# Optimization experiments

Measured on AMD Instinct MI355X. Metric: run time of the kernel, lower is better.

## Reference

```python
import jax, jax.numpy as jnp
import numpy as np

N_NODES = 12288
N_EDGES = 393216
LATENT = 128
EDGE_F = 4


def setup_inputs() -> dict:
    key = jax.random.key(0)
    k1, k2, k3, k4 = jax.random.split(key, 4)
    z = jax.random.normal(k1, (N_NODES, LATENT), dtype=jnp.float32)
    edge_index = jax.random.randint(k2, (2, N_EDGES), 0, N_NODES, dtype=jnp.int64)
    edge_attr = jax.random.normal(k3, (N_EDGES, EDGE_F), dtype=jnp.float32)
    W = jax.random.normal(k4, (1, 2 * LATENT), dtype=jnp.float32) * (1.0 / np.sqrt(2 * LATENT))
    b = jnp.zeros((1,), dtype=jnp.float32)
    return {"z": z, "edge_index": edge_index, "edge_attr": edge_attr, "W": W, "b": b}


def reference(z, edge_index, edge_attr, W, b):
    # z: [N, D], edge_index: [2, E], edge_attr: [E, F], W: [1, 2D], b: [1]
    num_nodes = z.shape[0]
    row, col = edge_index[0], edge_index[1]
    # gather node embeddings per edge and apply tiny linear: [E, 2D] @ [2D, 1]
    edge_features = jnp.concatenate([z[row], z[col]], axis=1)
    specified_edge_probs = (edge_features @ W.T + b)[:, 0]  # [E]
    # scatter edge probs into dense NxN (indexed assignment, like torch)
    full_edge_probs = jnp.zeros((num_nodes, num_nodes), dtype=z.dtype).at[row, col].set(specified_edge_probs)
    # to_dense_adj scatter-adds edge_attr -> [N, N, F]; sum(dim=3) commutes, so add summed attr
    adj = jnp.zeros((num_nodes, num_nodes), dtype=edge_attr.dtype).at[row, col].add(edge_attr.sum(axis=1))
    return adj + full_edge_probs
```

## Files before the change

kernel.cpp:

```cpp
#include <hip/hip_runtime.h>

#define N_NODES 12288
#define N_EDGES 393216
#define LATENT  128

#define E_BITS  19
#define E_MASK  ((1u << E_BITS) - 1u)

__device__ __forceinline__ unsigned int hash32(unsigned int key) {
    key ^= key >> 16; key *= 0x85ebca6bu;
    key ^= key >> 13; key *= 0xc2b2ae35u;
    key ^= key >> 16;
    return key;
}

__global__ void node_dots(const float* __restrict__ z, const float* __restrict__ W,
                          float* __restrict__ s1, float* __restrict__ s2) {
    int node = (int)((blockIdx.x * blockDim.x + threadIdx.x) >> 6);
    int lane = (int)(threadIdx.x & 63);
    if (node >= N_NODES) return;
    const float* zr = z + (size_t)node * LATENT;
    float a  = zr[lane];
    float bb = zr[lane + 64];
    float p1 = a * W[lane]       + bb * W[lane + 64];
    float p2 = a * W[lane + 128] + bb * W[lane + 192];
    #pragma unroll
    for (int off = 32; off > 0; off >>= 1) {
        p1 += __shfl_down(p1, off, 64);
        p2 += __shfl_down(p2, off, 64);
    }
    if (lane == 0) { s1[node] = p1; s2[node] = p2; }
}

__global__ void build_table(const int* __restrict__ ei,
                            unsigned long long* __restrict__ table,
                            unsigned int tab_mask) {
    int e = (int)(blockIdx.x * blockDim.x + threadIdx.x);
    if (e >= N_EDGES) return;
    unsigned int r = (unsigned int)ei[e];
    unsigned int c = (unsigned int)ei[e + N_EDGES];
    unsigned int key = r * (unsigned int)N_NODES + c;
    unsigned long long packed = (((unsigned long long)(key + 1u)) << E_BITS) | (unsigned int)e;
    unsigned int h = hash32(key) & tab_mask;
    for (;;) {
        unsigned long long old = atomicCAS(&table[h], 0ull, packed);
        if (old == 0ull) break;
        if ((unsigned int)(old >> E_BITS) == key + 1u) {
            atomicMax(&table[h], packed);
            break;
        }
        h = (h + 1u) & tab_mask;
    }
}

__global__ void scatter_edges(const int* __restrict__ ei, const float* __restrict__ ea,
                              const float* __restrict__ s1, const float* __restrict__ s2,
                              const float* __restrict__ bptr,
                              const unsigned long long* __restrict__ table,
                              unsigned int tab_mask,
                              float* __restrict__ out) {
    int e = (int)(blockIdx.x * blockDim.x + threadIdx.x);
    if (e >= N_EDGES) return;
    unsigned int r = (unsigned int)ei[e];
    unsigned int c = (unsigned int)ei[e + N_EDGES];
    unsigned int key = r * (unsigned int)N_NODES + c;
    float4 a4 = ((const float4*)ea)[e];
    float val = a4.x + a4.y + a4.z + a4.w;

    unsigned int h = hash32(key) & tab_mask;
    for (;;) {
        unsigned long long entry = table[h];
        if (entry == 0ull) break;
        if ((unsigned int)(entry >> E_BITS) == key + 1u) {
            if ((unsigned int)(entry & E_MASK) == (unsigned int)e)
                val += s1[r] + s2[c] + bptr[0];
            break;
        }
        h = (h + 1u) & tab_mask;
    }
    atomicAdd(&out[(size_t)key], val);
}

extern "C" void kernel_launch(void* const* d_in, const int* in_sizes, int n_in,
                              void* d_out, int out_size, void* d_ws, size_t ws_size,
                              hipStream_t stream) {
    const float* z  = (const float*)d_in[0];
    const int*   ei = (const int*)d_in[1];
    const float* ea = (const float*)d_in[2];
    const float* W  = (const float*)d_in[3];
    const float* b  = (const float*)d_in[4];
    float* out = (float*)d_out;

    char* ws = (char*)d_ws;
    float* s1 = (float*)ws;
    float* s2 = (float*)(ws + (size_t)N_NODES * sizeof(float));
    unsigned long long* table = (unsigned long long*)(ws + 2ull * N_NODES * sizeof(float));
    size_t head = 2ull * N_NODES * sizeof(float);

    int bits = 19;
    while (bits < 22 && head + (8ull << (bits + 1)) <= ws_size) bits++;
    unsigned int tab_mask = (1u << bits) - 1u;
    size_t tab_bytes = 8ull << bits;

    hipMemsetAsync(d_out, 0, (size_t)out_size * sizeof(float), stream);
    hipMemsetAsync(table, 0, tab_bytes, stream);

    node_dots<<<N_NODES / 4, 256, 0, stream>>>(z, W, s1, s2);
    build_table<<<N_EDGES / 256, 256, 0, stream>>>(ei, table, tab_mask);
    scatter_edges<<<N_EDGES / 256, 256, 0, stream>>>(ei, ea, s1, s2, b, table, tab_mask, out);
}
```

Measured before the change: 670.3 us.

## Fuse attr scatter into table build and add probs via table sweep

The edge-attribute atomic scatter moves into the hash-table build kernel. The old second per-edge pass, which re-read the edges and re-probed the hash table, is replaced by a linear sweep over the table that adds each unique edge's probability to the output with a plain read-modify-write. This drops one pass over edge_index and edge_attr along with the random table probes. The table is capped at 2^20 entries, which shortens the sweep but raises load factor and collision chains compared with the old larger table.

```diff
diff --git a/kernel.cpp b/kernel.cpp
--- a/kernel.cpp
+++ b/kernel.cpp
@@ -32,14 +32,18 @@
     if (lane == 0) { s1[node] = p1; s2[node] = p2; }
 }
 
-__global__ void build_table(const int* __restrict__ ei,
-                            unsigned long long* __restrict__ table,
-                            unsigned int tab_mask) {
+__global__ void edge_pass(const int* __restrict__ ei, const float* __restrict__ ea,
+                          unsigned long long* __restrict__ table, unsigned int tab_mask,
+                          float* __restrict__ out) {
     int e = (int)(blockIdx.x * blockDim.x + threadIdx.x);
     if (e >= N_EDGES) return;
     unsigned int r = (unsigned int)ei[e];
     unsigned int c = (unsigned int)ei[e + N_EDGES];
     unsigned int key = r * (unsigned int)N_NODES + c;
+
+    float4 a4 = ((const float4*)ea)[e];
+    atomicAdd(&out[(size_t)key], a4.x + a4.y + a4.z + a4.w);
+
     unsigned long long packed = (((unsigned long long)(key + 1u)) << E_BITS) | (unsigned int)e;
     unsigned int h = hash32(key) & tab_mask;
     for (;;) {
@@ -53,32 +57,17 @@
     }
 }
 
-__global__ void scatter_edges(const int* __restrict__ ei, const float* __restrict__ ea,
-                              const float* __restrict__ s1, const float* __restrict__ s2,
-                              const float* __restrict__ bptr,
-                              const unsigned long long* __restrict__ table,
-                              unsigned int tab_mask,
-                              float* __restrict__ out) {
-    int e = (int)(blockIdx.x * blockDim.x + threadIdx.x);
-    if (e >= N_EDGES) return;
-    unsigned int r = (unsigned int)ei[e];
-    unsigned int c = (unsigned int)ei[e + N_EDGES];
-    unsigned int key = r * (unsigned int)N_NODES + c;
-    float4 a4 = ((const float4*)ea)[e];
-    float val = a4.x + a4.y + a4.z + a4.w;
-
-    unsigned int h = hash32(key) & tab_mask;
-    for (;;) {
-        unsigned long long entry = table[h];
-        if (entry == 0ull) break;
-        if ((unsigned int)(entry >> E_BITS) == key + 1u) {
-            if ((unsigned int)(entry & E_MASK) == (unsigned int)e)
-                val += s1[r] + s2[c] + bptr[0];
-            break;
-        }
-        h = (h + 1u) & tab_mask;
-    }
-    atomicAdd(&out[(size_t)key], val);
+__global__ void add_probs(const unsigned long long* __restrict__ table, unsigned int tab_n,
+                          const float* __restrict__ s1, const float* __restrict__ s2,
+                          const float* __restrict__ bptr, float* __restrict__ out) {
+    unsigned int i = blockIdx.x * blockDim.x + threadIdx.x;
+    if (i >= tab_n) return;
+    unsigned long long entry = table[i];
+    if (entry == 0ull) return;
+    unsigned int key = (unsigned int)(entry >> E_BITS) - 1u;
+    unsigned int r = key / (unsigned int)N_NODES;
+    unsigned int c = key - r * (unsigned int)N_NODES;
+    out[(size_t)key] += s1[r] + s2[c] + bptr[0];
 }
 
 extern "C" void kernel_launch(void* const* d_in, const int* in_sizes, int n_in,
@@ -97,15 +86,15 @@
     unsigned long long* table = (unsigned long long*)(ws + 2ull * N_NODES * sizeof(float));
     size_t head = 2ull * N_NODES * sizeof(float);
 
-    int bits = 19;
-    while (bits < 22 && head + (8ull << (bits + 1)) <= ws_size) bits++;
-    unsigned int tab_mask = (1u << bits) - 1u;
+    int bits = (head + (8ull << 20) <= ws_size) ? 20 : 19;
+    unsigned int tab_n = 1u << bits;
+    unsigned int tab_mask = tab_n - 1u;
     size_t tab_bytes = 8ull << bits;
 
     hipMemsetAsync(d_out, 0, (size_t)out_size * sizeof(float), stream);
     hipMemsetAsync(table, 0, tab_bytes, stream);
 
     node_dots<<<N_NODES / 4, 256, 0, stream>>>(z, W, s1, s2);
-    build_table<<<N_EDGES / 256, 256, 0, stream>>>(ei, table, tab_mask);
-    scatter_edges<<<N_EDGES / 256, 256, 0, stream>>>(ei, ea, s1, s2, b, table, tab_mask, out);
+    edge_pass<<<N_EDGES / 256, 256, 0, stream>>>(ei, ea, table, tab_mask, out);
+    add_probs<<<tab_n / 256, 256, 0, stream>>>(table, tab_n, s1, s2, b, out);
 }
```

After: 683.7 us. +2.0%, slower.
